# Performance work log

Hardware: AMD Instinct MI355X
Metric: run time of the kernel (lower is better)

The kernel has to match this reference:

```python
import jax, jax.numpy as jnp
import numpy as np

BATCH, SEQ, FEAT, UNITS, OUT = 128, 2048, 64, 64, 6


def setup_inputs() -> dict:
    key = jax.random.key(0)
    ks = jax.random.split(key, 12)
    s = 0.05
    inp = {
        "x": jax.random.normal(ks[0], (BATCH, SEQ, FEAT), dtype=jnp.float32),
        # LSTMCell 0 (kernel, recurrent_kernel, bias); gate order i,f,g,o
        "W0": jax.random.normal(ks[1], (FEAT, 4 * UNITS), dtype=jnp.float32) * s,
        "U0": jax.random.normal(ks[2], (UNITS, 4 * UNITS), dtype=jnp.float32) * s,
        "b0": jax.random.normal(ks[3], (4 * UNITS,), dtype=jnp.float32) * s,
        # LSTMCell 1 (shared by layers 2 AND 3, as in the original code)
        "W1": jax.random.normal(ks[4], (UNITS, 4 * UNITS), dtype=jnp.float32) * s,
        "U1": jax.random.normal(ks[5], (UNITS, 4 * UNITS), dtype=jnp.float32) * s,
        "b1": jax.random.normal(ks[6], (4 * UNITS,), dtype=jnp.float32) * s,
        # Dense heads
        "Wf": jax.random.normal(ks[7], (UNITS, 64), dtype=jnp.float32) * s,
        "bf": jax.random.normal(ks[8], (64,), dtype=jnp.float32) * s,
        "Wo": jax.random.normal(ks[9], (64, OUT), dtype=jnp.float32) * s,
        "bo": jax.random.normal(ks[10], (OUT,), dtype=jnp.float32) * s,
    }
    return inp


def _lstm_cell(c, h, xin, W, U, b):
    # Keras LSTMCell math, gate order i, f, g(candidate), o
    z = xin @ W + h @ U + b  # [B, 4U]
    i, f, g, o = jnp.split(z, 4, axis=-1)
    c_new = jax.nn.sigmoid(f) * c + jax.nn.sigmoid(i) * jnp.tanh(g)
    h_new = jax.nn.sigmoid(o) * jnp.tanh(c_new)
    return c_new, h_new


def reference(x, W0, U0, b0, W1, U1, b1, Wf, bf, Wo, bo):
    B = x.shape[0]
    z = jnp.zeros((B, UNITS), dtype=x.dtype)
    init = (z, z, z, z, z, z)  # (c0,h0,c1,h1,c2,h2)

    def step(carry, xt):
        c0, h0, c1, h1, c2, h2 = carry
        c0, h0 = _lstm_cell(c0, h0, xt, W0, U0, b0)
        c1, h1 = _lstm_cell(c1, h1, h0, W1, U1, b1)
        # NOTE: original code reuses rnn_cell1's weights for the 3rd layer
        c2, h2 = _lstm_cell(c2, h2, h1, W1, U1, b1)
        return (c0, h0, c1, h1, c2, h2), None

    xt = jnp.swapaxes(x, 0, 1)  # [T, B, F]
    (c0, h0, c1, h1, c2, h2), _ = jax.lax.scan(step, init, xt)
    y = jax.nn.relu(h2 @ Wf + bf)
    return y @ Wo + bo
```

## Files before the change

kernel.cpp:

```cpp
#include <hip/hip_runtime.h>

#define BATCHN 128
#define SEQT   2048
#define FEAT   64
#define UNITS  64
#define NCOL   256
#define OUTD   6

typedef __fp16 hv2 __attribute__((ext_vector_type(2)));

__device__ __forceinline__ float fast_exp2(float x) {
#if __has_builtin(__builtin_amdgcn_exp2f)
    return __builtin_amdgcn_exp2f(x);
#else
    return exp2f(x);
#endif
}
__device__ __forceinline__ float fast_rcp(float x) {
#if __has_builtin(__builtin_amdgcn_rcpf)
    return __builtin_amdgcn_rcpf(x);
#else
    return 1.0f / x;
#endif
}
__device__ __forceinline__ float sig_(float x) {
    return fast_rcp(1.0f + fast_exp2(-1.4426950408889634f * x));
}
__device__ __forceinline__ float tanh_(float x) {
    float e = fast_exp2(-2.8853900817779268f * x);
    return fmaf(2.0f, fast_rcp(1.0f + e), -1.0f);
}

__device__ __forceinline__ float fdot2_(hv2 a, hv2 b, float c) {
#if __has_builtin(__builtin_amdgcn_fdot2)
    return __builtin_amdgcn_fdot2(a, b, c, false);
#else
    return fmaf((float)a.x, (float)b.x, fmaf((float)a.y, (float)b.y, c));
#endif
}
__device__ __forceinline__ hv2 cvtpk_(float a, float b) {
    return __builtin_amdgcn_cvt_pkrtz(a, b);
}
__device__ __forceinline__ unsigned int rlane_(unsigned int v, int l) {
    return (unsigned int)__builtin_amdgcn_readlane((int)v, l);
}
__device__ __forceinline__ float bperm_(int byteaddr, float v) {
    return __builtin_bit_cast(float,
        __builtin_amdgcn_ds_bpermute(byteaddr, __builtin_bit_cast(int, v)));
}

__global__ __launch_bounds__(192, 1)
void lstm3_w3(const float* __restrict__ x,
              const float* __restrict__ W0, const float* __restrict__ U0,
              const float* __restrict__ b0,
              const float* __restrict__ W1, const float* __restrict__ U1,
              const float* __restrict__ b1,
              const float* __restrict__ Wf, const float* __restrict__ bfv,
              const float* __restrict__ Wo, const float* __restrict__ bov,
              float* __restrict__ out)
{
    const int b   = blockIdx.x;
    const int tid = threadIdx.x;
    const int g   = tid >> 6;
    const int u   = tid & 63;
    const int j32 = u & 31;

    __shared__ unsigned int lhp[3][2][32];
    __shared__ float lh2f[UNITS];
    __shared__ float lact[UNITS];

    const float* Wsel = (g == 0) ? W0 : W1;
    const float* Usel = (g == 0) ? U0 : U1;
    const float* bsel = (g == 0) ? b0 : b1;

    hv2 wF[32][4], wR[32][4];
    float biasv[4];
#pragma unroll
    for (int gg = 0; gg < 4; ++gg) {
        const int col = (gg << 6) + u;
#pragma unroll
        for (int j = 0; j < 32; ++j) {
            hv2 f, r;
            f.x = (__fp16)Wsel[(2 * j) * NCOL + col];
            f.y = (__fp16)Wsel[(2 * j + 1) * NCOL + col];
            r.x = (__fp16)Usel[(2 * j) * NCOL + col];
            r.y = (__fp16)Usel[(2 * j + 1) * NCOL + col];
            wF[j][gg] = f;
            wR[j][gg] = r;
        }
        biasv[gg] = bsel[col];
    }

    ((unsigned int*)lhp)[tid] = 0u;

    const float2* x2 = (const float2*)(x + (size_t)b * SEQT * FEAT);
    float2 xrA = {0.f, 0.f}, xrB = {0.f, 0.f};
    if (g == 0 && u < 32) {
        xrA = x2[0 * 32 + u];
        xrB = x2[1 * 32 + u];
    }
    __syncthreads();

    float c = 0.f, h = 0.f;
    unsigned int rpk = 0u;

#define TICK(TK, XR)                                                          \
    {                                                                         \
        const int p_ = (TK) & 1;                                              \
        const int t_ = (TK) - g;                                              \
        const float2 xcur = XR;                                               \
        if (g == 0 && u < 32) {     \
            int tn = (TK) + 2; if (tn > SEQT - 1) tn = SEQT - 1;              \
            XR = x2[(size_t)tn * 32 + u];                                     \
        }                                                                     \
        if (t_ >= 0 && t_ < SEQT) {                                           \
            unsigned int ffpk;                                                \
            if (g == 0) ffpk = __builtin_bit_cast(unsigned int,               \
                                                  cvtpk_(xcur.x, xcur.y));    \
            else        ffpk = lhp[g - 1][p_ ^ 1][j32];    \
            float a0A = 0.f, a0B = 0.f, a1A = 0.f, a1B = 0.f;                 \
            float a2A = 0.f, a2B = 0.f, a3A = 0.f, a3B = 0.f;                 \
            _Pragma("unroll")                                                 \
            for (int j = 0; j < 32; j += 2) {                                 \
                hv2 r0 = __builtin_bit_cast(hv2, rlane_(rpk, j));             \
                hv2 r1 = __builtin_bit_cast(hv2, rlane_(rpk, j + 1));         \
                a0A = fdot2_(r0, wR[j][0], a0A);                              \
                a1A = fdot2_(r0, wR[j][1], a1A);                              \
                a2A = fdot2_(r0, wR[j][2], a2A);                              \
                a3A = fdot2_(r0, wR[j][3], a3A);                              \
                a0B = fdot2_(r1, wR[j + 1][0], a0B);                          \
                a1B = fdot2_(r1, wR[j + 1][1], a1B);                          \
                a2B = fdot2_(r1, wR[j + 1][2], a2B);                          \
                a3B = fdot2_(r1, wR[j + 1][3], a3B);                          \
            }                                                                 \
            _Pragma("unroll")                                                 \
            for (int j = 0; j < 32; j += 2) {                                 \
                hv2 f0 = __builtin_bit_cast(hv2, rlane_(ffpk, j));            \
                hv2 f1 = __builtin_bit_cast(hv2, rlane_(ffpk, j + 1));        \
                a0A = fdot2_(f0, wF[j][0], a0A);                              \
                a1A = fdot2_(f0, wF[j][1], a1A);                              \
                a2A = fdot2_(f0, wF[j][2], a2A);                              \
                a3A = fdot2_(f0, wF[j][3], a3A);                              \
                a0B = fdot2_(f1, wF[j + 1][0], a0B);                          \
                a1B = fdot2_(f1, wF[j + 1][1], a1B);                          \
                a2B = fdot2_(f1, wF[j + 1][2], a2B);                          \
                a3B = fdot2_(f1, wF[j + 1][3], a3B);                          \
            }                                                                 \
            const float zi = a0A + a0B + biasv[0];                            \
            const float zf = a1A + a1B + biasv[1];                            \
            const float zg = a2A + a2B + biasv[2];                            \
            const float zo = a3A + a3B + biasv[3];                            \
            const float ig = sig_(zi), fg = sig_(zf);                         \
            const float gv = tanh_(zg), og = sig_(zo);                        \
            c = fg * c + ig * gv;                                             \
            h = og * tanh_(c);                                                \
            const float h0 = bperm_(j32 * 8,     h);             \
            const float h1 = bperm_(j32 * 8 + 4, h);             \
            rpk = __builtin_bit_cast(unsigned int, cvtpk_(h0, h1));           \
            if (u < 32) lhp[g][p_][u] = rpk;                  \
            if (g == 2 && t_ == SEQT - 1) lh2f[u] = h;                        \
        }                                                                     \
        asm volatile("s_waitcnt lgkmcnt(0)\n\ts_barrier" ::: "memory");       \
    }

    for (int tk = 0; tk < SEQT + 2; tk += 2) {
        TICK(tk,     xrA)
        TICK(tk + 1, xrB)
    }
#undef TICK

    __syncthreads();

    if (tid < UNITS) {
        float a = bfv[tid];
#pragma unroll
        for (int k = 0; k < UNITS; ++k) a += lh2f[k] * Wf[k * 64 + tid];
        lact[tid] = fmaxf(a, 0.f);
    }
    __syncthreads();
    if (tid < OUTD) {
        float a = bov[tid];
#pragma unroll
        for (int k = 0; k < UNITS; ++k) a += lact[k] * Wo[k * OUTD + tid];
        out[b * OUTD + tid] = a;
    }
}

extern "C" void kernel_launch(void* const* d_in, const int* in_sizes, int n_in,
                              void* d_out, int out_size, void* d_ws, size_t ws_size,
                              hipStream_t stream) {
    const float* x   = (const float*)d_in[0];
    const float* W0  = (const float*)d_in[1];
    const float* U0  = (const float*)d_in[2];
    const float* b0  = (const float*)d_in[3];
    const float* W1  = (const float*)d_in[4];
    const float* U1  = (const float*)d_in[5];
    const float* b1  = (const float*)d_in[6];
    const float* Wf  = (const float*)d_in[7];
    const float* bfv = (const float*)d_in[8];
    const float* Wo  = (const float*)d_in[9];
    const float* bov = (const float*)d_in[10];
    float* out = (float*)d_out;

    lstm3_w3<<<BATCHN, 192, 0, stream>>>(x, W0, U0, b0, W1, U1, b1,
                                         Wf, bfv, Wo, bov, out);
}
```

Baseline: 1.925 ms.

## Split input and recurrent projections into separate pipelined waves per layer

Each LSTM layer now uses two wavefronts: one computes the input projection (plus bias) one tick ahead and passes the gate pre-activations through LDS, while the other adds the recurrent projection and applies the cell update. This halves the dependent dot-product chain on the recurrent critical path and halves per-thread weight registers. It costs an extra LDS round trip per step, barriers across six waves instead of three, and a deeper pipeline with more warm-up ticks.

```diff
diff --git a/kernel.cpp b/kernel.cpp
--- a/kernel.cpp
+++ b/kernel.cpp
@@ -49,121 +49,122 @@
         __builtin_amdgcn_ds_bpermute(byteaddr, __builtin_bit_cast(int, v)));
 }
 
-__global__ __launch_bounds__(192, 1)
-void lstm3_w3(const float* __restrict__ x,
-              const float* __restrict__ W0, const float* __restrict__ U0,
-              const float* __restrict__ b0,
-              const float* __restrict__ W1, const float* __restrict__ U1,
-              const float* __restrict__ b1,
-              const float* __restrict__ Wf, const float* __restrict__ bfv,
-              const float* __restrict__ Wo, const float* __restrict__ bov,
-              float* __restrict__ out)
+__global__ __launch_bounds__(384, 2)
+void lstm3_ffrec(const float* __restrict__ x,
+                 const float* __restrict__ W0, const float* __restrict__ U0,
+                 const float* __restrict__ b0,
+                 const float* __restrict__ W1, const float* __restrict__ U1,
+                 const float* __restrict__ b1,
+                 const float* __restrict__ Wf, const float* __restrict__ bfv,
+                 const float* __restrict__ Wo, const float* __restrict__ bov,
+                 float* __restrict__ out)
 {
     const int b   = blockIdx.x;
     const int tid = threadIdx.x;
-    const int g   = tid >> 6;
+    const int wid = tid >> 6;
+    const int g   = wid >> 1;
+    const int r   = wid & 1;
     const int u   = tid & 63;
     const int j32 = u & 31;
 
     __shared__ unsigned int lhp[3][2][32];
+    __shared__ __align__(16) float lzf[3][2][UNITS][4];
     __shared__ float lh2f[UNITS];
     __shared__ float lact[UNITS];
 
-    const float* Wsel = (g == 0) ? W0 : W1;
-    const float* Usel = (g == 0) ? U0 : U1;
+    const float* M = (g == 0) ? ((r == 0) ? W0 : U0) : ((r == 0) ? W1 : U1);
     const float* bsel = (g == 0) ? b0 : b1;
 
-    hv2 wF[32][4], wR[32][4];
+    hv2 wM[32][4];
     float biasv[4];
 #pragma unroll
     for (int gg = 0; gg < 4; ++gg) {
         const int col = (gg << 6) + u;
 #pragma unroll
         for (int j = 0; j < 32; ++j) {
-            hv2 f, r;
-            f.x = (__fp16)Wsel[(2 * j) * NCOL + col];
-            f.y = (__fp16)Wsel[(2 * j + 1) * NCOL + col];
-            r.x = (__fp16)Usel[(2 * j) * NCOL + col];
-            r.y = (__fp16)Usel[(2 * j + 1) * NCOL + col];
-            wF[j][gg] = f;
-            wR[j][gg] = r;
+            hv2 w;
+            w.x = (__fp16)M[(2 * j) * NCOL + col];
+            w.y = (__fp16)M[(2 * j + 1) * NCOL + col];
+            wM[j][gg] = w;
         }
         biasv[gg] = bsel[col];
     }
 
-    ((unsigned int*)lhp)[tid] = 0u;
+    if (tid < 192) ((unsigned int*)lhp)[tid] = 0u;
+    for (int i = tid; i < 3 * 2 * UNITS * 4; i += 384) ((float*)lzf)[i] = 0.f;
 
     const float2* x2 = (const float2*)(x + (size_t)b * SEQT * FEAT);
     float2 xrA = {0.f, 0.f}, xrB = {0.f, 0.f};
-    if (g == 0 && u < 32) {
+    if (wid == 0 && u < 32) {
         xrA = x2[0 * 32 + u];
         xrB = x2[1 * 32 + u];
     }
     __syncthreads();
 
+    const int alpha = 2 * g + r;
     float c = 0.f, h = 0.f;
     unsigned int rpk = 0u;
 
 #define TICK(TK, XR)                                                          \
     {                                                                         \
-        const int p_ = (TK) & 1;                                              \
-        const int t_ = (TK) - g;                                              \
+        const int t_ = (TK) - alpha;                                          \
         const float2 xcur = XR;                                               \
-        if (g == 0 && u < 32) {     \
+        if (wid == 0 && u < 32) {                    \
             int tn = (TK) + 2; if (tn > SEQT - 1) tn = SEQT - 1;              \
             XR = x2[(size_t)tn * 32 + u];                                     \
         }                                                                     \
         if (t_ >= 0 && t_ < SEQT) {                                           \
-            unsigned int ffpk;                                                \
-            if (g == 0) ffpk = __builtin_bit_cast(unsigned int,               \
-                                                  cvtpk_(xcur.x, xcur.y));    \
-            else        ffpk = lhp[g - 1][p_ ^ 1][j32];    \
-            float a0A = 0.f, a0B = 0.f, a1A = 0.f, a1B = 0.f;                 \
-            float a2A = 0.f, a2B = 0.f, a3A = 0.f, a3B = 0.f;                 \
+            const int p_ = t_ & 1;                                            \
+            unsigned int srcpk;                                               \
+            float4 zin = {0.f, 0.f, 0.f, 0.f};                                \
+            if (r == 0) {                                                     \
+                srcpk = (g == 0) ? __builtin_bit_cast(unsigned int,           \
+                                                      cvtpk_(xcur.x, xcur.y)) \
+                                 : lhp[g - 1][p_][j32];            \
+            } else {                                                          \
+                srcpk = rpk;                                                  \
+                zin = *(const float4*)&lzf[g][p_][u][0];          \
+            }                                                                 \
+            float aA0, aA1, aA2, aA3;                                         \
+            if (r == 0) { aA0 = biasv[0]; aA1 = biasv[1];                     \
+                          aA2 = biasv[2]; aA3 = biasv[3]; }                   \
+            else        { aA0 = zin.x; aA1 = zin.y;                           \
+                          aA2 = zin.z; aA3 = zin.w; }                         \
+            float aB0 = 0.f, aB1 = 0.f, aB2 = 0.f, aB3 = 0.f;                 \
             _Pragma("unroll")                                                 \
             for (int j = 0; j < 32; j += 2) {                                 \
-                hv2 r0 = __builtin_bit_cast(hv2, rlane_(rpk, j));             \
-                hv2 r1 = __builtin_bit_cast(hv2, rlane_(rpk, j + 1));         \
-                a0A = fdot2_(r0, wR[j][0], a0A);                              \
-                a1A = fdot2_(r0, wR[j][1], a1A);                              \
-                a2A = fdot2_(r0, wR[j][2], a2A);                              \
-                a3A = fdot2_(r0, wR[j][3], a3A);                              \
-                a0B = fdot2_(r1, wR[j + 1][0], a0B);                          \
-                a1B = fdot2_(r1, wR[j + 1][1], a1B);                          \
-                a2B = fdot2_(r1, wR[j + 1][2], a2B);                          \
-                a3B = fdot2_(r1, wR[j + 1][3], a3B);                          \
+                hv2 p0 = __builtin_bit_cast(hv2, rlane_(srcpk, j));           \
+                hv2 p1 = __builtin_bit_cast(hv2, rlane_(srcpk, j + 1));       \
+                aA0 = fdot2_(p0, wM[j][0], aA0);                              \
+                aA1 = fdot2_(p0, wM[j][1], aA1);                              \
+                aA2 = fdot2_(p0, wM[j][2], aA2);                              \
+                aA3 = fdot2_(p0, wM[j][3], aA3);                              \
+                aB0 = fdot2_(p1, wM[j + 1][0], aB0);                          \
+                aB1 = fdot2_(p1, wM[j + 1][1], aB1);                          \
+                aB2 = fdot2_(p1, wM[j + 1][2], aB2);                          \
+                aB3 = fdot2_(p1, wM[j + 1][3], aB3);                          \
             }                                                                 \
-            _Pragma("unroll")                                                 \
-            for (int j = 0; j < 32; j += 2) {                                 \
-                hv2 f0 = __builtin_bit_cast(hv2, rlane_(ffpk, j));            \
-                hv2 f1 = __builtin_bit_cast(hv2, rlane_(ffpk, j + 1));        \
-                a0A = fdot2_(f0, wF[j][0], a0A);                              \
-                a1A = fdot2_(f0, wF[j][1], a1A);                              \
-                a2A = fdot2_(f0, wF[j][2], a2A);                              \
-                a3A = fdot2_(f0, wF[j][3], a3A);                              \
-                a0B = fdot2_(f1, wF[j + 1][0], a0B);                          \
-                a1B = fdot2_(f1, wF[j + 1][1], a1B);                          \
-                a2B = fdot2_(f1, wF[j + 1][2], a2B);                          \
-                a3B = fdot2_(f1, wF[j + 1][3], a3B);                          \
+            if (r == 0) {                                \
+                float4 z4 = {aA0 + aB0, aA1 + aB1, aA2 + aB2, aA3 + aB3};     \
+                *(float4*)&lzf[g][p_][u][0] = z4;                             \
+            } else {                                \
+                const float zi = aA0 + aB0, zf = aA1 + aB1;                   \
+                const float zg = aA2 + aB2, zo = aA3 + aB3;                   \
+                const float ig = sig_(zi), fg = sig_(zf);                     \
+                const float gv = tanh_(zg), og = sig_(zo);                    \
+                c = fg * c + ig * gv;                                         \
+                h = og * tanh_(c);                                            \
+                const float h0 = bperm_(j32 * 8,     h);                      \
+                const float h1 = bperm_(j32 * 8 + 4, h);                      \
+                rpk = __builtin_bit_cast(unsigned int, cvtpk_(h0, h1));       \
+                if (u < 32) lhp[g][p_][u] = rpk;                              \
+                if (g == 2 && t_ == SEQT - 1) lh2f[u] = h;                    \
             }                                                                 \
-            const float zi = a0A + a0B + biasv[0];                            \
-            const float zf = a1A + a1B + biasv[1];                            \
-            const float zg = a2A + a2B + biasv[2];                            \
-            const float zo = a3A + a3B + biasv[3];                            \
-            const float ig = sig_(zi), fg = sig_(zf);                         \
-            const float gv = tanh_(zg), og = sig_(zo);                        \
-            c = fg * c + ig * gv;                                             \
-            h = og * tanh_(c);                                                \
-            const float h0 = bperm_(j32 * 8,     h);             \
-            const float h1 = bperm_(j32 * 8 + 4, h);             \
-            rpk = __builtin_bit_cast(unsigned int, cvtpk_(h0, h1));           \
-            if (u < 32) lhp[g][p_][u] = rpk;                  \
-            if (g == 2 && t_ == SEQT - 1) lh2f[u] = h;                        \
         }                                                                     \
         asm volatile("s_waitcnt lgkmcnt(0)\n\ts_barrier" ::: "memory");       \
     }
 
-    for (int tk = 0; tk < SEQT + 2; tk += 2) {
+    for (int tk = 0; tk < SEQT + 6; tk += 2) {
         TICK(tk,     xrA)
         TICK(tk + 1, xrB)
     }
@@ -202,6 +203,6 @@
     const float* bov = (const float*)d_in[10];
     float* out = (float*)d_out;
 
-    lstm3_w3<<<BATCHN, 192, 0, stream>>>(x, W0, U0, b0, W1, U1, b1,
-                                         Wf, bfv, Wo, bov, out);
-}
+    lstm3_ffrec<<<BATCHN, 384, 0, stream>>>(x, W0, U0, b0, W1, U1, b1,
+                                            Wf, bfv, Wo, bov, out);
+}
```

Result: faster. 1.885 ms (-2.1%).
